# Optimization experiments

Hardware: AMD Instinct MI355X
Metric: run time of the kernel (lower is better)

Reference implementation:

```python
import jax, jax.numpy as jnp
import numpy as np

B, C, CI, H, W = 8, 256, 128, 64, 64
EPS = 1e-5


def conv1x1(x, w, b):
    # x: [B,C,H,W], w: [O,C], b: [O] -> [B,O,H,W]
    return jnp.einsum('bchw,oc->bohw', x, w) + b[None, :, None, None]


def maxpool2(x):
    # 2x2 max pool, stride 2 (NCHW)
    b, c, h, w = x.shape
    return x.reshape(b, c, h // 2, 2, w // 2, 2).max(axis=(3, 5))


def setup_inputs() -> dict:
    key = jax.random.key(0)
    ks = jax.random.split(key, 14)
    s_in = 1.0 / np.sqrt(C)
    s_ci = 1.0 / np.sqrt(CI)
    return {
        'x': jax.random.normal(ks[0], (B, C, H, W), jnp.float32),
        'w_theta': jax.random.normal(ks[1], (CI, C), jnp.float32) * s_in,
        'b_theta': jax.random.normal(ks[2], (CI,), jnp.float32) * 0.01,
        'w_phi': jax.random.normal(ks[3], (CI, C), jnp.float32) * s_in,
        'b_phi': jax.random.normal(ks[4], (CI,), jnp.float32) * 0.01,
        'w_g': jax.random.normal(ks[5], (CI, C), jnp.float32) * s_in,
        'b_g': jax.random.normal(ks[6], (CI,), jnp.float32) * 0.01,
        'w_w': jax.random.normal(ks[7], (C, CI), jnp.float32) * s_ci,
        'b_w': jax.random.normal(ks[8], (C,), jnp.float32) * 0.01,
        'bn_gamma': jax.random.normal(ks[9], (C,), jnp.float32) * 0.1,
        'bn_beta': jax.random.normal(ks[10], (C,), jnp.float32) * 0.1,
        'bn_mean': jax.random.normal(ks[11], (C,), jnp.float32) * 0.1,
        'bn_var': jax.random.uniform(ks[12], (C,), jnp.float32) + 0.5,
    }


def reference(x, w_theta, b_theta, w_phi, b_phi, w_g, b_g,
              w_w, b_w, bn_gamma, bn_beta, bn_mean, bn_var):
    b = x.shape[0]
    theta_x = conv1x1(x, w_theta, b_theta).reshape(b, CI, -1)            # [B,Ci,N]
    phi_x = maxpool2(conv1x1(x, w_phi, b_phi)).reshape(b, CI, -1)        # [B,Ci,M]
    g_x = maxpool2(conv1x1(x, w_g, b_g)).reshape(b, CI, -1)              # [B,Ci,M]
    m = phi_x.shape[-1]
    # unnormalized attention: f = theta^T phi / M  -> [B,N,M]
    f = jnp.einsum('bcn,bcm->bnm', theta_x, phi_x) / m
    y = jnp.einsum('bnm,bcm->bcn', f, g_x).reshape(b, CI, H, W)          # [B,Ci,H,W]
    w_y = conv1x1(y, w_w, b_w)                                           # [B,C,H,W]
    inv = jax.lax.rsqrt(bn_var + EPS)
    bn = (w_y - bn_mean[None, :, None, None]) * (bn_gamma * inv)[None, :, None, None] \
         + bn_beta[None, :, None, None]
    return bn + x
```

## Files before the change

kernel.cpp:

```cpp
#include <hip/hip_runtime.h>


typedef __attribute__((ext_vector_type(8))) short bf16x8;
typedef __attribute__((ext_vector_type(4))) float f32x4;
typedef unsigned short u16;
typedef unsigned int u32;

constexpr int Bn = 8, Cc = 256, CiC = 128, NnC = 4096, MmC = 1024;
constexpr float kEps = 1e-5f;

__device__ __forceinline__ u16 f2b(float f) {
  u32 u = __float_as_uint(f);
  return (u16)((u + 0x7fffu + ((u >> 16) & 1u)) >> 16);
}
__device__ __forceinline__ float b2f(u16 h) {
  return __uint_as_float(((u32)h) << 16);
}
__device__ __forceinline__ u32 pack2(float a, float b) {
  return (u32)f2b(a) | ((u32)f2b(b) << 16);
}
__device__ __forceinline__ void gl16(const void* g, void* l) {
  __builtin_amdgcn_global_load_lds(
      (const __attribute__((address_space(1))) void*)g,
      (__attribute__((address_space(3))) void*)l, 16, 0, 0);
}

__global__ __launch_bounds__(256) void prepw_kernel(
    const float* __restrict__ wt, const float* __restrict__ wp,
    const float* __restrict__ wg, const float* __restrict__ ww,
    u16* __restrict__ W3b, u16* __restrict__ Wwb) {
  const int idx = blockIdx.x * 256 + threadIdx.x;
  if (idx < 98304) {
    const int r = idx >> 8, c = idx & 255;
    const float v = (r < 128)   ? wt[r * 256 + c]
                    : (r < 256) ? wp[(r - 128) * 256 + c]
                                : wg[(r - 256) * 256 + c];
    W3b[idx] = f2b(v);
  } else {
    const int j = idx - 98304;
    Wwb[j] = f2b(ww[j]);
  }
}

__global__ __launch_bounds__(256) void prepx_kernel(const float* __restrict__ x,
                                                    u16* __restrict__ xT) {
  __shared__ float sm[64][65];
  const int b = blockIdx.z, c0 = blockIdx.y * 64, n0 = blockIdx.x * 64;
  const int tid = threadIdx.x;
  {
    const int n = tid & 63, cg = tid >> 6;
#pragma unroll
    for (int i = 0; i < 16; ++i) {
      const int c = cg * 16 + i;
      sm[c][n] = x[((size_t)(b * Cc + c0 + c)) * NnC + n0 + n];
    }
  }
  __syncthreads();
  {
    const int n = tid >> 2, q = tid & 3;
    u16 v[16];
#pragma unroll
    for (int j = 0; j < 16; ++j) v[j] = f2b(sm[q * 16 + j][n]);
    uint4 o0, o1;
    o0.x = v[0] | ((u32)v[1] << 16);
    o0.y = v[2] | ((u32)v[3] << 16);
    o0.z = v[4] | ((u32)v[5] << 16);
    o0.w = v[6] | ((u32)v[7] << 16);
    o1.x = v[8] | ((u32)v[9] << 16);
    o1.y = v[10] | ((u32)v[11] << 16);
    o1.z = v[12] | ((u32)v[13] << 16);
    o1.w = v[14] | ((u32)v[15] << 16);
    uint4* dst = (uint4*)(xT + ((size_t)(b * NnC + n0 + n)) * Cc + c0 + q * 16);
    dst[0] = o0;
    dst[1] = o1;
  }
}

__global__ __launch_bounds__(256) void conv3_kernel(
    const u16* __restrict__ xT, const u16* __restrict__ W3b,
    const float* __restrict__ b_theta, const float* __restrict__ b_phi,
    const float* __restrict__ b_g, u16* __restrict__ thetaT,
    u16* __restrict__ phiT, u16* __restrict__ gP) {
  __shared__ u16 sm[2][2][8192];
  const int mt = blockIdx.x, nt = blockIdx.y, b = blockIdx.z;
  const int n0 = nt * 128;
  const int tid = threadIdx.x;
  const int w = tid >> 6, lane = tid & 63;
  const int r16 = lane & 15, kg = lane >> 4;
  const int oh = (w & 1) * 64, nh = (w >> 1) * 64;

  auto stage = [&](int buf, int k0) {
#pragma unroll
    for (int i = 0; i < 4; ++i) {
      const int lin = i * 4096 + tid * 16;
      const int row = lin >> 7, byte = lin & 127;
      gl16((const char*)W3b + (size_t)(mt * 128 + row) * 512 + k0 * 2 +
               (byte ^ ((row & 7) << 4)),
           (char*)&sm[buf][0][0] + lin);
    }
#pragma unroll
    for (int i = 0; i < 4; ++i) {
      const int lin = i * 4096 + tid * 16;
      const int row = lin >> 7, byte = lin & 127;
      gl16((const char*)xT + ((size_t)(b * NnC + n0 + row) * Cc + k0) * 2 +
               (byte ^ ((row & 7) << 4)),
           (char*)&sm[buf][1][0] + lin);
    }
  };

  f32x4 acc[4][4];
#pragma unroll
  for (int i = 0; i < 4; ++i)
#pragma unroll
    for (int j = 0; j < 4; ++j) acc[i][j] = (f32x4)0.f;

  stage(0, 0);
  __syncthreads();
  for (int kt = 0; kt < 4; ++kt) {
    if (kt < 3) stage((kt + 1) & 1, (kt + 1) * 64);
    const char* A = (const char*)&sm[kt & 1][0][0];
    const char* Bm = (const char*)&sm[kt & 1][1][0];
#pragma unroll
    for (int ks = 0; ks < 2; ++ks) {
      bf16x8 af[4], bfr[4];
#pragma unroll
      for (int f = 0; f < 4; ++f) {
        const int o = oh + f * 16 + r16;
        af[f] = *(const bf16x8*)(A + ((o * 128 + ks * 64 + kg * 16) ^
                                      ((o & 7) << 4)));
        const int n = nh + f * 16 + r16;
        bfr[f] = *(const bf16x8*)(Bm + ((n * 128 + ks * 64 + kg * 16) ^
                                        ((n & 7) << 4)));
      }
#pragma unroll
      for (int fo = 0; fo < 4; ++fo)
#pragma unroll
        for (int fn = 0; fn < 4; ++fn)
          acc[fo][fn] = __builtin_amdgcn_mfma_f32_16x16x32_bf16(
              af[fo], bfr[fn], acc[fo][fn], 0, 0, 0);
    }
    __syncthreads();
  }

  const float* bias = (mt == 0) ? b_theta : (mt == 1) ? b_phi : b_g;
  u16* ldst = (u16*)&sm[0][0][0];
#pragma unroll
  for (int fo = 0; fo < 4; ++fo) {
    const int obase = oh + fo * 16 + kg * 4;
    const float b0 = bias[obase], b1 = bias[obase + 1], b2 = bias[obase + 2],
                b3 = bias[obase + 3];
#pragma unroll
    for (int fn = 0; fn < 4; ++fn) {
      const int n = nh + fn * 16 + r16;
      const f32x4 v = acc[fo][fn];
      uint2 p;
      p.x = pack2(v.x + b0, v.y + b1);
      p.y = pack2(v.z + b2, v.w + b3);
      *(uint2*)((char*)ldst + ((n * 256 + obase * 2) ^ ((n & 7) << 4))) = p;
    }
  }
  __syncthreads();

  if (mt == 0) {
#pragma unroll
    for (int i = 0; i < 8; ++i) {
      const int lin = i * 4096 + tid * 16;
      const int nl = lin >> 8, byte = lin & 255;
      const uint4 v =
          *(const uint4*)((const char*)ldst + ((nl * 256 + byte) ^ ((nl & 7) << 4)));
      *(uint4*)((char*)thetaT + (size_t)(b * NnC + n0 + nl) * CiC * 2 + byte) = v;
    }
  } else if (mt == 1) {
    const int ci = tid & 127, mg = tid >> 7;
#pragma unroll
    for (int i = 0; i < 16; ++i) {
      const int mw = mg * 16 + i;
      const int n00 = 2 * mw;
      float v0 = b2f(*(const u16*)((const char*)ldst +
                                   ((n00 * 256 + ci * 2) ^ ((n00 & 7) << 4))));
      float v1 = b2f(*(const u16*)((const char*)ldst +
                                   (((n00 + 1) * 256 + ci * 2) ^ (((n00 + 1) & 7) << 4))));
      float v2 = b2f(*(const u16*)((const char*)ldst +
                                   (((n00 + 64) * 256 + ci * 2) ^ (((n00 + 64) & 7) << 4))));
      float v3 = b2f(*(const u16*)((const char*)ldst +
                                   (((n00 + 65) * 256 + ci * 2) ^ (((n00 + 65) & 7) << 4))));
      const float mx = fmaxf(fmaxf(v0, v1), fmaxf(v2, v3));
      phiT[((size_t)(b * MmC + nt * 32 + mw)) * CiC + ci] = f2b(mx);
    }
  } else {
    const int ci = tid >> 1, half = tid & 1;
#pragma unroll
    for (int i = 0; i < 16; ++i) {
      const int mw = half * 16 + i;
      const int n00 = 2 * mw;
      float v0 = b2f(*(const u16*)((const char*)ldst +
                                   ((n00 * 256 + ci * 2) ^ ((n00 & 7) << 4))));
      float v1 = b2f(*(const u16*)((const char*)ldst +
                                   (((n00 + 1) * 256 + ci * 2) ^ (((n00 + 1) & 7) << 4))));
      float v2 = b2f(*(const u16*)((const char*)ldst +
                                   (((n00 + 64) * 256 + ci * 2) ^ (((n00 + 64) & 7) << 4))));
      float v3 = b2f(*(const u16*)((const char*)ldst +
                                   (((n00 + 65) * 256 + ci * 2) ^ (((n00 + 65) & 7) << 4))));
      const float mx = fmaxf(fmaxf(v0, v1), fmaxf(v2, v3));
      gP[((size_t)(b * CiC + ci)) * MmC + nt * 32 + mw] = f2b(mx);
    }
  }
}

__global__ __launch_bounds__(512) void attn_kernel(
    const u16* __restrict__ thetaT, const u16* __restrict__ phiT,
    const u16* __restrict__ gP, u16* __restrict__ yT) {
  __shared__ u16 thS[128 * 128];
  __shared__ u16 phS[2][64 * 128];
  __shared__ u16 gS[2][128 * 64];
  __shared__ u16 SP[128 * 64];
  const int nt = blockIdx.x, b = blockIdx.y;
  const int n0 = nt * 128;
  const int tid = threadIdx.x, w = tid >> 6, lane = tid & 63;
  const int r16 = lane & 15, kg = lane >> 4;

#pragma unroll
  for (int i = 0; i < 4; ++i) {
    const int lin = i * 8192 + tid * 16;
    const int nl = lin >> 8, byte = lin & 255;
    gl16((const char*)thetaT + (size_t)(b * NnC + n0 + nl) * CiC * 2 +
             (byte ^ ((nl & 7) << 4)),
         (char*)thS + lin);
  }
  auto stagePG = [&](int buf, int m0) {
#pragma unroll
    for (int i = 0; i < 2; ++i) {
      const int lin = i * 8192 + tid * 16;
      const int ml = lin >> 8, byte = lin & 255;
      gl16((const char*)phiT + (size_t)(b * MmC + m0 + ml) * CiC * 2 +
               (byte ^ ((ml & 7) << 4)),
           (char*)&phS[buf][0] + lin);
    }
#pragma unroll
    for (int i = 0; i < 2; ++i) {
      const int lin = i * 8192 + tid * 16;
      const int cil = lin >> 7, byte = lin & 127;
      gl16((const char*)gP + ((size_t)(b * CiC + cil) * MmC + m0) * 2 +
               (byte ^ ((cil & 7) << 4)),
           (char*)&gS[buf][0] + lin);
    }
  };
  stagePG(0, 0);
  __syncthreads();

  f32x4 accY[2][4];
#pragma unroll
  for (int i = 0; i < 2; ++i)
#pragma unroll
    for (int j = 0; j < 4; ++j) accY[i][j] = (f32x4)0.f;

  const int mrow = (w >> 1) * 16 + r16;
  const int nbs = (w & 1) * 64;
  const int mcb = (w >> 1) * 16 + kg * 4;
  const int cib = (w & 3) * 32;
  const int nb2 = (w >> 2) * 64;

  for (int mi = 0; mi < 16; ++mi) {
    const int cur = mi & 1;
    if (mi < 15) stagePG(cur ^ 1, (mi + 1) * 64);
    const char* ph = (const char*)&phS[cur][0];
    f32x4 s[4];
#pragma unroll
    for (int nf = 0; nf < 4; ++nf) s[nf] = (f32x4)0.f;
#pragma unroll
    for (int ks = 0; ks < 4; ++ks) {
      const bf16x8 af = *(const bf16x8*)(ph + ((mrow * 256 + ks * 64 + kg * 16) ^
                                               ((mrow & 7) << 4)));
#pragma unroll
      for (int nf = 0; nf < 4; ++nf) {
        const int n = nbs + nf * 16 + r16;
        const bf16x8 bf_ = *(const bf16x8*)((const char*)thS +
                                            ((n * 256 + ks * 64 + kg * 16) ^
                                             ((n & 7) << 4)));
        s[nf] = __builtin_amdgcn_mfma_f32_16x16x32_bf16(af, bf_, s[nf], 0, 0, 0);
      }
    }
#pragma unroll
    for (int nf = 0; nf < 4; ++nf) {
      const int n = nbs + nf * 16 + r16;
      uint2 p;
      p.x = pack2(s[nf].x, s[nf].y);
      p.y = pack2(s[nf].z, s[nf].w);
      *(uint2*)((char*)SP + ((n * 128 + mcb * 2) ^ ((n & 7) << 4))) = p;
    }
    __syncthreads();
    const char* gs = (const char*)&gS[cur][0];
#pragma unroll
    for (int ks2 = 0; ks2 < 2; ++ks2) {
      bf16x8 ga[2];
#pragma unroll
      for (int cf = 0; cf < 2; ++cf) {
        const int ci = cib + cf * 16 + r16;
        ga[cf] = *(const bf16x8*)(gs + ((ci * 128 + ks2 * 64 + kg * 16) ^
                                        ((ci & 7) << 4)));
      }
#pragma unroll
      for (int nf = 0; nf < 4; ++nf) {
        const int n = nb2 + nf * 16 + r16;
        const bf16x8 sb = *(const bf16x8*)((const char*)SP +
                                           ((n * 128 + ks2 * 64 + kg * 16) ^
                                            ((n & 7) << 4)));
#pragma unroll
        for (int cf = 0; cf < 2; ++cf)
          accY[cf][nf] = __builtin_amdgcn_mfma_f32_16x16x32_bf16(
              ga[cf], sb, accY[cf][nf], 0, 0, 0);
      }
    }
    __syncthreads();
  }

  constexpr float scl = 1.f / (float)MmC;
  u16* yt = thS;
#pragma unroll
  for (int cf = 0; cf < 2; ++cf) {
    const int c0 = cib + cf * 16 + kg * 4;
#pragma unroll
    for (int nf = 0; nf < 4; ++nf) {
      const int n = nb2 + nf * 16 + r16;
      const f32x4 v = accY[cf][nf];
      uint2 p;
      p.x = pack2(v.x * scl, v.y * scl);
      p.y = pack2(v.z * scl, v.w * scl);
      *(uint2*)((char*)yt + ((n * 256 + c0 * 2) ^ ((n & 7) << 4))) = p;
    }
  }
  __syncthreads();
#pragma unroll
  for (int i = 0; i < 4; ++i) {
    const int lin = i * 8192 + tid * 16;
    const int nl = lin >> 8, byte = lin & 255;
    const uint4 v =
        *(const uint4*)((const char*)yt + ((nl * 256 + byte) ^ ((nl & 7) << 4)));
    *(uint4*)((char*)yT + (size_t)(b * NnC + n0 + nl) * CiC * 2 + byte) = v;
  }
}

__global__ __launch_bounds__(256) void convw_kernel(
    const u16* __restrict__ yT, const u16* __restrict__ Wwb,
    const float* __restrict__ b_w, const float* __restrict__ gamma,
    const float* __restrict__ beta, const float* __restrict__ mean,
    const float* __restrict__ var, const float* __restrict__ x,
    float* __restrict__ out) {
  __shared__ u16 smA[128 * 128];
  __shared__ u16 smB[128 * 128];
  __shared__ float scs[128], offs[128];
  const int mt = blockIdx.x, nt = blockIdx.y, b = blockIdx.z;
  const int n0 = nt * 128, tid = threadIdx.x;
  const int w = tid >> 6, lane = tid & 63;
  const int r16 = lane & 15, kg = lane >> 4;
  if (tid < 128) {
    const int o = mt * 128 + tid;
    const float sc = gamma[o] * rsqrtf(var[o] + kEps);
    scs[tid] = sc;
    offs[tid] = beta[o] + (b_w[o] - mean[o]) * sc;
  }
#pragma unroll
  for (int i = 0; i < 8; ++i) {
    const int lin = i * 4096 + tid * 16;
    const int row = lin >> 8, byte = lin & 255;
    gl16((const char*)Wwb + (size_t)(mt * 128 + row) * 256 +
             (byte ^ ((row & 7) << 4)),
         (char*)smA + lin);
    gl16((const char*)yT + (size_t)(b * NnC + n0 + row) * 256 +
             (byte ^ ((row & 7) << 4)),
         (char*)smB + lin);
  }
  __syncthreads();

  f32x4 acc[4][4];
#pragma unroll
  for (int i = 0; i < 4; ++i)
#pragma unroll
    for (int j = 0; j < 4; ++j) acc[i][j] = (f32x4)0.f;
  const int oh = (w & 1) * 64, nh = (w >> 1) * 64;
#pragma unroll
  for (int ks = 0; ks < 4; ++ks) {
    bf16x8 af[4], bfr[4];
#pragma unroll
    for (int f = 0; f < 4; ++f) {
      const int o = oh + f * 16 + r16;
      af[f] = *(const bf16x8*)((const char*)smA +
                               ((o * 256 + ks * 64 + kg * 16) ^ ((o & 7) << 4)));
      const int n = nh + f * 16 + r16;
      bfr[f] = *(const bf16x8*)((const char*)smB +
                                ((n * 256 + ks * 64 + kg * 16) ^ ((n & 7) << 4)));
    }
#pragma unroll
    for (int fo = 0; fo < 4; ++fo)
#pragma unroll
      for (int fn = 0; fn < 4; ++fn)
        acc[fo][fn] = __builtin_amdgcn_mfma_f32_16x16x32_bf16(
            af[fo], bfr[fn], acc[fo][fn], 0, 0, 0);
  }

  const size_t xb = ((size_t)b * Cc + mt * 128) * NnC;
#pragma unroll
  for (int fo = 0; fo < 4; ++fo) {
#pragma unroll
    for (int r = 0; r < 4; ++r) {
      const int ol = oh + fo * 16 + kg * 4 + r;
      const float sc = scs[ol], of = offs[ol];
      const size_t rowoff = xb + (size_t)ol * NnC + n0;
#pragma unroll
      for (int fn = 0; fn < 4; ++fn) {
        const int n = nh + fn * 16 + r16;
        out[rowoff + n] = fmaf(acc[fo][fn][r], sc, of) + x[rowoff + n];
      }
    }
  }
}

extern "C" void kernel_launch(void* const* d_in, const int* in_sizes, int n_in,
                              void* d_out, int out_size, void* d_ws,
                              size_t ws_size, hipStream_t stream) {
  const float* x = (const float*)d_in[0];
  const float* w_theta = (const float*)d_in[1];
  const float* b_theta = (const float*)d_in[2];
  const float* w_phi = (const float*)d_in[3];
  const float* b_phi = (const float*)d_in[4];
  const float* w_g = (const float*)d_in[5];
  const float* b_g = (const float*)d_in[6];
  const float* w_w = (const float*)d_in[7];
  const float* b_w = (const float*)d_in[8];
  const float* bn_gamma = (const float*)d_in[9];
  const float* bn_beta = (const float*)d_in[10];
  const float* bn_mean = (const float*)d_in[11];
  const float* bn_var = (const float*)d_in[12];
  float* out = (float*)d_out;

  char* ws = (char*)d_ws;
  u16* xT = (u16*)ws;
  u16* thetaT = (u16*)(ws + 16777216);
  u16* phiT = (u16*)(ws + 25165824);
  u16* gP = (u16*)(ws + 27262976);
  u16* yT = (u16*)(ws + 29360128);
  u16* W3b = (u16*)(ws + 37748736);
  u16* Wwb = (u16*)(ws + 37945344);
  if (ws_size < 38010880ull) return;

  prepw_kernel<<<dim3(512), dim3(256), 0, stream>>>(w_theta, w_phi, w_g, w_w,
                                                    W3b, Wwb);
  prepx_kernel<<<dim3(64, 4, 8), dim3(256), 0, stream>>>(x, xT);
  conv3_kernel<<<dim3(3, 32, 8), dim3(256), 0, stream>>>(
      xT, W3b, b_theta, b_phi, b_g, thetaT, phiT, gP);
  attn_kernel<<<dim3(32, 8), dim3(512), 0, stream>>>(thetaT, phiT, gP, yT);
  convw_kernel<<<dim3(2, 32, 8), dim3(256), 0, stream>>>(
      yT, Wwb, b_w, bn_gamma, bn_beta, bn_mean, bn_var, x, out);
}
```

Baseline: 165.0 us.

## Reassociate linear attention into per-batch folded weight matrix applied to x

```diff
diff --git a/kernel.cpp b/kernel.cpp
--- a/kernel.cpp
+++ b/kernel.cpp
@@ -6,7 +6,7 @@
 typedef unsigned short u16;
 typedef unsigned int u32;
 
-constexpr int Bn = 8, Cc = 256, CiC = 128, NnC = 4096, MmC = 1024;
+constexpr int Cc = 256, NnC = 4096;
 constexpr float kEps = 1e-5f;
 
 __device__ __forceinline__ u16 f2b(float f) {
@@ -26,20 +26,11 @@
 }
 
 __global__ __launch_bounds__(256) void prepw_kernel(
-    const float* __restrict__ wt, const float* __restrict__ wp,
-    const float* __restrict__ wg, const float* __restrict__ ww,
-    u16* __restrict__ W3b, u16* __restrict__ Wwb) {
+    const float* __restrict__ wp, const float* __restrict__ wg,
+    u16* __restrict__ Wfg) {
   const int idx = blockIdx.x * 256 + threadIdx.x;
-  if (idx < 98304) {
-    const int r = idx >> 8, c = idx & 255;
-    const float v = (r < 128)   ? wt[r * 256 + c]
-                    : (r < 256) ? wp[(r - 128) * 256 + c]
-                                : wg[(r - 256) * 256 + c];
-    W3b[idx] = f2b(v);
-  } else {
-    const int j = idx - 98304;
-    Wwb[j] = f2b(ww[j]);
-  }
+  const int r = idx >> 8, c = idx & 255;
+  Wfg[idx] = f2b(r < 128 ? wp[r * 256 + c] : wg[(r - 128) * 256 + c]);
 }
 
 __global__ __launch_bounds__(256) void prepx_kernel(const float* __restrict__ x,
@@ -76,11 +67,10 @@
   }
 }
 
-__global__ __launch_bounds__(256) void conv3_kernel(
-    const u16* __restrict__ xT, const u16* __restrict__ W3b,
-    const float* __restrict__ b_theta, const float* __restrict__ b_phi,
-    const float* __restrict__ b_g, u16* __restrict__ thetaT,
-    u16* __restrict__ phiT, u16* __restrict__ gP) {
+__global__ __launch_bounds__(256) void convfg_kernel(
+    const u16* __restrict__ xT, const u16* __restrict__ Wfg,
+    const float* __restrict__ b_phi, const float* __restrict__ b_g,
+    u16* __restrict__ phiT, u16* __restrict__ gT) {
   __shared__ u16 sm[2][2][8192];
   const int mt = blockIdx.x, nt = blockIdx.y, b = blockIdx.z;
   const int n0 = nt * 128;
@@ -94,7 +84,7 @@
     for (int i = 0; i < 4; ++i) {
       const int lin = i * 4096 + tid * 16;
       const int row = lin >> 7, byte = lin & 127;
-      gl16((const char*)W3b + (size_t)(mt * 128 + row) * 512 + k0 * 2 +
+      gl16((const char*)Wfg + (size_t)(mt * 128 + row) * 512 + k0 * 2 +
                (byte ^ ((row & 7) << 4)),
            (char*)&sm[buf][0][0] + lin);
     }
@@ -142,7 +132,7 @@
     __syncthreads();
   }
 
-  const float* bias = (mt == 0) ? b_theta : (mt == 1) ? b_phi : b_g;
+  const float* bias = (mt == 0) ? b_phi : b_g;
   u16* ldst = (u16*)&sm[0][0][0];
 #pragma unroll
   for (int fo = 0; fo < 4; ++fo) {
@@ -161,241 +151,242 @@
   }
   __syncthreads();
 
-  if (mt == 0) {
+  u16* dst = (mt == 0) ? phiT : gT;
+  const int ci = tid >> 1, half = tid & 1;
+#pragma unroll
+  for (int i = 0; i < 16; ++i) {
+    const int mw = half * 16 + i;
+    const int n00 = 2 * mw;
+    float v0 = b2f(*(const u16*)((const char*)ldst +
+                                 ((n00 * 256 + ci * 2) ^ ((n00 & 7) << 4))));
+    float v1 = b2f(*(const u16*)((const char*)ldst +
+                                 (((n00 + 1) * 256 + ci * 2) ^ (((n00 + 1) & 7) << 4))));
+    float v2 = b2f(*(const u16*)((const char*)ldst +
+                                 (((n00 + 64) * 256 + ci * 2) ^ (((n00 + 64) & 7) << 4))));
+    float v3 = b2f(*(const u16*)((const char*)ldst +
+                                 (((n00 + 65) * 256 + ci * 2) ^ (((n00 + 65) & 7) << 4))));
+    const float mx = fmaxf(fmaxf(v0, v1), fmaxf(v2, v3));
+    dst[((size_t)(b * 128 + ci)) * 1024 + nt * 32 + mw] = f2b(mx);
+  }
+}
+
+__global__ __launch_bounds__(256) void g2_kernel(const u16* __restrict__ phiT,
+                                                 const u16* __restrict__ gT,
+                                                 float* __restrict__ A_g2) {
+  __shared__ u16 sm[2][12288];
+  const int ch0 = blockIdx.x * 64, b = blockIdx.y;
+  const int tid = threadIdx.x;
+  const int w = tid >> 6, lane = tid & 63;
+  const int r16 = lane & 15, kg = lane >> 4;
+  const int cih = (w & 1) * 64, cch = (w >> 1) * 32;
+
+  auto stage = [&](int buf, int m0) {
+#pragma unroll
+    for (int i = 0; i < 4; ++i) {
+      const int lin = i * 4096 + tid * 16;
+      const int row = lin >> 7, byte = lin & 127;
+      gl16((const char*)gT + ((size_t)(b * 128 + row) * 1024 + m0) * 2 +
+               (byte ^ ((row & 7) << 4)),
+           (char*)&sm[buf][0] + lin);
+    }
+#pragma unroll
+    for (int i = 0; i < 2; ++i) {
+      const int lin = i * 4096 + tid * 16;
+      const int row = lin >> 7, byte = lin & 127;
+      gl16((const char*)phiT + ((size_t)(b * 128 + ch0 + row) * 1024 + m0) * 2 +
+               (byte ^ ((row & 7) << 4)),
+           (char*)&sm[buf][8192] + lin);
+    }
+  };
+
+  f32x4 acc[4][2];
+#pragma unroll
+  for (int i = 0; i < 4; ++i)
+#pragma unroll
+    for (int j = 0; j < 2; ++j) acc[i][j] = (f32x4)0.f;
+
+  stage(0, 0);
+  __syncthreads();
+  for (int kt = 0; kt < 16; ++kt) {
+    if (kt < 15) stage((kt + 1) & 1, (kt + 1) * 64);
+    const char* A = (const char*)&sm[kt & 1][0];
+    const char* Bp = A + 16384;
+#pragma unroll
+    for (int ks = 0; ks < 2; ++ks) {
+      bf16x8 af[4], bfr[2];
+#pragma unroll
+      for (int f = 0; f < 4; ++f) {
+        const int o = cih + f * 16 + r16;
+        af[f] = *(const bf16x8*)(A + ((o * 128 + ks * 64 + kg * 16) ^
+                                      ((o & 7) << 4)));
+      }
+#pragma unroll
+      for (int f = 0; f < 2; ++f) {
+        const int lc = cch + f * 16 + r16;
+        bfr[f] = *(const bf16x8*)(Bp + ((lc * 128 + ks * 64 + kg * 16) ^
+                                        ((lc & 7) << 4)));
+      }
+#pragma unroll
+      for (int fo = 0; fo < 4; ++fo)
+#pragma unroll
+        for (int fn = 0; fn < 2; ++fn)
+          acc[fo][fn] = __builtin_amdgcn_mfma_f32_16x16x32_bf16(
+              af[fo], bfr[fn], acc[fo][fn], 0, 0, 0);
+    }
+    __syncthreads();
+  }
+
+  constexpr float scl = 1.f / 1024.f;
+#pragma unroll
+  for (int fo = 0; fo < 4; ++fo) {
+#pragma unroll
+    for (int r = 0; r < 4; ++r) {
+      const int ci = cih + fo * 16 + kg * 4 + r;
+#pragma unroll
+      for (int fn = 0; fn < 2; ++fn) {
+        const int c = ch0 + cch + fn * 16 + r16;
+        A_g2[(size_t)b * 16384 + ci * 128 + c] = acc[fo][fn][r] * scl;
+      }
+    }
+  }
+}
+
+__global__ __launch_bounds__(256) void t1_kernel(const float* __restrict__ A_g2,
+                                                 const float* __restrict__ w_theta,
+                                                 float* __restrict__ T1) {
+  __shared__ float As[16][128];
+  __shared__ float Ws[128][17];
+  const int tile = blockIdx.x, b = blockIdx.y;
+  const int ci0 = (tile >> 4) * 16, j0 = (tile & 15) * 16;
+  const int t = threadIdx.x;
+#pragma unroll
+  for (int i = 0; i < 8; ++i) {
+    const int idx = t + i * 256;
+    As[idx >> 7][idx & 127] =
+        A_g2[(size_t)b * 16384 + (ci0 + (idx >> 7)) * 128 + (idx & 127)];
+    Ws[idx >> 4][idx & 15] = w_theta[(idx >> 4) * 256 + j0 + (idx & 15)];
+  }
+  __syncthreads();
+  const int tci = t >> 4, tj = t & 15;
+  float s = 0.f;
+#pragma unroll 8
+  for (int c = 0; c < 128; ++c) s = fmaf(As[tci][c], Ws[c][tj], s);
+  T1[(size_t)b * 32768 + (ci0 + tci) * 256 + j0 + tj] = s;
+}
+
+__global__ __launch_bounds__(256) void wbig_kernel(
+    const float* __restrict__ T1, const float* __restrict__ A_g2,
+    const float* __restrict__ w_w, const float* __restrict__ b_theta,
+    const float* __restrict__ b_w, u16* __restrict__ Wbig,
+    float* __restrict__ beff) {
+  __shared__ float Ws2[16][128];
+  __shared__ float T1s[128][17];
+  __shared__ float v1[128];
+  const int tile = blockIdx.x, b = blockIdx.y;
+  const int t = threadIdx.x;
+  if (tile < 256) {
+    const int o0 = (tile >> 4) * 16, j0 = (tile & 15) * 16;
 #pragma unroll
     for (int i = 0; i < 8; ++i) {
-      const int lin = i * 4096 + tid * 16;
-      const int nl = lin >> 8, byte = lin & 255;
-      const uint4 v =
-          *(const uint4*)((const char*)ldst + ((nl * 256 + byte) ^ ((nl & 7) << 4)));
-      *(uint4*)((char*)thetaT + (size_t)(b * NnC + n0 + nl) * CiC * 2 + byte) = v;
-    }
-  } else if (mt == 1) {
-    const int ci = tid & 127, mg = tid >> 7;
-#pragma unroll
-    for (int i = 0; i < 16; ++i) {
-      const int mw = mg * 16 + i;
-      const int n00 = 2 * mw;
-      float v0 = b2f(*(const u16*)((const char*)ldst +
-                                   ((n00 * 256 + ci * 2) ^ ((n00 & 7) << 4))));
-      float v1 = b2f(*(const u16*)((const char*)ldst +
-                                   (((n00 + 1) * 256 + ci * 2) ^ (((n00 + 1) & 7) << 4))));
-      float v2 = b2f(*(const u16*)((const char*)ldst +
-                                   (((n00 + 64) * 256 + ci * 2) ^ (((n00 + 64) & 7) << 4))));
-      float v3 = b2f(*(const u16*)((const char*)ldst +
-                                   (((n00 + 65) * 256 + ci * 2) ^ (((n00 + 65) & 7) << 4))));
-      const float mx = fmaxf(fmaxf(v0, v1), fmaxf(v2, v3));
-      phiT[((size_t)(b * MmC + nt * 32 + mw)) * CiC + ci] = f2b(mx);
-    }
+      const int idx = t + i * 256;
+      Ws2[idx >> 7][idx & 127] = w_w[(o0 + (idx >> 7)) * 128 + (idx & 127)];
+      T1s[idx >> 4][idx & 15] =
+          T1[(size_t)b * 32768 + (idx >> 4) * 256 + j0 + (idx & 15)];
+    }
+    __syncthreads();
+    const int to = t >> 4, tj = t & 15;
+    float s = 0.f;
+#pragma unroll 8
+    for (int c = 0; c < 128; ++c) s = fmaf(Ws2[to][c], T1s[c][tj], s);
+    Wbig[(size_t)b * 65536 + (o0 + to) * 256 + j0 + tj] = f2b(s);
   } else {
-    const int ci = tid >> 1, half = tid & 1;
-#pragma unroll
-    for (int i = 0; i < 16; ++i) {
-      const int mw = half * 16 + i;
-      const int n00 = 2 * mw;
-      float v0 = b2f(*(const u16*)((const char*)ldst +
-                                   ((n00 * 256 + ci * 2) ^ ((n00 & 7) << 4))));
-      float v1 = b2f(*(const u16*)((const char*)ldst +
-                                   (((n00 + 1) * 256 + ci * 2) ^ (((n00 + 1) & 7) << 4))));
-      float v2 = b2f(*(const u16*)((const char*)ldst +
-                                   (((n00 + 64) * 256 + ci * 2) ^ (((n00 + 64) & 7) << 4))));
-      float v3 = b2f(*(const u16*)((const char*)ldst +
-                                   (((n00 + 65) * 256 + ci * 2) ^ (((n00 + 65) & 7) << 4))));
-      const float mx = fmaxf(fmaxf(v0, v1), fmaxf(v2, v3));
-      gP[((size_t)(b * CiC + ci)) * MmC + nt * 32 + mw] = f2b(mx);
-    }
-  }
-}
-
-__global__ __launch_bounds__(512) void attn_kernel(
-    const u16* __restrict__ thetaT, const u16* __restrict__ phiT,
-    const u16* __restrict__ gP, u16* __restrict__ yT) {
-  __shared__ u16 thS[128 * 128];
-  __shared__ u16 phS[2][64 * 128];
-  __shared__ u16 gS[2][128 * 64];
-  __shared__ u16 SP[128 * 64];
-  const int nt = blockIdx.x, b = blockIdx.y;
-  const int n0 = nt * 128;
-  const int tid = threadIdx.x, w = tid >> 6, lane = tid & 63;
-  const int r16 = lane & 15, kg = lane >> 4;
-
-#pragma unroll
-  for (int i = 0; i < 4; ++i) {
-    const int lin = i * 8192 + tid * 16;
-    const int nl = lin >> 8, byte = lin & 255;
-    gl16((const char*)thetaT + (size_t)(b * NnC + n0 + nl) * CiC * 2 +
-             (byte ^ ((nl & 7) << 4)),
-         (char*)thS + lin);
-  }
-  auto stagePG = [&](int buf, int m0) {
-#pragma unroll
-    for (int i = 0; i < 2; ++i) {
-      const int lin = i * 8192 + tid * 16;
-      const int ml = lin >> 8, byte = lin & 255;
-      gl16((const char*)phiT + (size_t)(b * MmC + m0 + ml) * CiC * 2 +
-               (byte ^ ((ml & 7) << 4)),
-           (char*)&phS[buf][0] + lin);
-    }
-#pragma unroll
-    for (int i = 0; i < 2; ++i) {
-      const int lin = i * 8192 + tid * 16;
-      const int cil = lin >> 7, byte = lin & 127;
-      gl16((const char*)gP + ((size_t)(b * CiC + cil) * MmC + m0) * 2 +
-               (byte ^ ((cil & 7) << 4)),
-           (char*)&gS[buf][0] + lin);
-    }
-  };
-  stagePG(0, 0);
-  __syncthreads();
-
-  f32x4 accY[2][4];
-#pragma unroll
-  for (int i = 0; i < 2; ++i)
-#pragma unroll
-    for (int j = 0; j < 4; ++j) accY[i][j] = (f32x4)0.f;
-
-  const int mrow = (w >> 1) * 16 + r16;
-  const int nbs = (w & 1) * 64;
-  const int mcb = (w >> 1) * 16 + kg * 4;
-  const int cib = (w & 3) * 32;
-  const int nb2 = (w >> 2) * 64;
-
-  for (int mi = 0; mi < 16; ++mi) {
-    const int cur = mi & 1;
-    if (mi < 15) stagePG(cur ^ 1, (mi + 1) * 64);
-    const char* ph = (const char*)&phS[cur][0];
-    f32x4 s[4];
-#pragma unroll
-    for (int nf = 0; nf < 4; ++nf) s[nf] = (f32x4)0.f;
-#pragma unroll
-    for (int ks = 0; ks < 4; ++ks) {
-      const bf16x8 af = *(const bf16x8*)(ph + ((mrow * 256 + ks * 64 + kg * 16) ^
-                                               ((mrow & 7) << 4)));
-#pragma unroll
-      for (int nf = 0; nf < 4; ++nf) {
-        const int n = nbs + nf * 16 + r16;
-        const bf16x8 bf_ = *(const bf16x8*)((const char*)thS +
-                                            ((n * 256 + ks * 64 + kg * 16) ^
-                                             ((n & 7) << 4)));
-        s[nf] = __builtin_amdgcn_mfma_f32_16x16x32_bf16(af, bf_, s[nf], 0, 0, 0);
-      }
-    }
-#pragma unroll
-    for (int nf = 0; nf < 4; ++nf) {
-      const int n = nbs + nf * 16 + r16;
-      uint2 p;
-      p.x = pack2(s[nf].x, s[nf].y);
-      p.y = pack2(s[nf].z, s[nf].w);
-      *(uint2*)((char*)SP + ((n * 128 + mcb * 2) ^ ((n & 7) << 4))) = p;
+    if (t < 128) {
+      float s = 0.f;
+      for (int c = 0; c < 128; ++c)
+        s = fmaf(A_g2[(size_t)b * 16384 + t * 128 + c], b_theta[c], s);
+      v1[t] = s;
     }
     __syncthreads();
-    const char* gs = (const char*)&gS[cur][0];
-#pragma unroll
-    for (int ks2 = 0; ks2 < 2; ++ks2) {
-      bf16x8 ga[2];
-#pragma unroll
-      for (int cf = 0; cf < 2; ++cf) {
-        const int ci = cib + cf * 16 + r16;
-        ga[cf] = *(const bf16x8*)(gs + ((ci * 128 + ks2 * 64 + kg * 16) ^
-                                        ((ci & 7) << 4)));
-      }
-#pragma unroll
-      for (int nf = 0; nf < 4; ++nf) {
-        const int n = nb2 + nf * 16 + r16;
-        const bf16x8 sb = *(const bf16x8*)((const char*)SP +
-                                           ((n * 128 + ks2 * 64 + kg * 16) ^
-                                            ((n & 7) << 4)));
-#pragma unroll
-        for (int cf = 0; cf < 2; ++cf)
-          accY[cf][nf] = __builtin_amdgcn_mfma_f32_16x16x32_bf16(
-              ga[cf], sb, accY[cf][nf], 0, 0, 0);
-      }
-    }
-    __syncthreads();
-  }
-
-  constexpr float scl = 1.f / (float)MmC;
-  u16* yt = thS;
-#pragma unroll
-  for (int cf = 0; cf < 2; ++cf) {
-    const int c0 = cib + cf * 16 + kg * 4;
-#pragma unroll
-    for (int nf = 0; nf < 4; ++nf) {
-      const int n = nb2 + nf * 16 + r16;
-      const f32x4 v = accY[cf][nf];
-      uint2 p;
-      p.x = pack2(v.x * scl, v.y * scl);
-      p.y = pack2(v.z * scl, v.w * scl);
-      *(uint2*)((char*)yt + ((n * 256 + c0 * 2) ^ ((n & 7) << 4))) = p;
-    }
-  }
-  __syncthreads();
-#pragma unroll
-  for (int i = 0; i < 4; ++i) {
-    const int lin = i * 8192 + tid * 16;
-    const int nl = lin >> 8, byte = lin & 255;
-    const uint4 v =
-        *(const uint4*)((const char*)yt + ((nl * 256 + byte) ^ ((nl & 7) << 4)));
-    *(uint4*)((char*)yT + (size_t)(b * NnC + n0 + nl) * CiC * 2 + byte) = v;
-  }
-}
-
-__global__ __launch_bounds__(256) void convw_kernel(
-    const u16* __restrict__ yT, const u16* __restrict__ Wwb,
-    const float* __restrict__ b_w, const float* __restrict__ gamma,
+    float s2 = b_w[t];
+    for (int ci = 0; ci < 128; ++ci) s2 = fmaf(w_w[t * 128 + ci], v1[ci], s2);
+    beff[b * 256 + t] = s2;
+  }
+}
+
+__global__ __launch_bounds__(256) void final_kernel(
+    const u16* __restrict__ xT, const u16* __restrict__ Wbig,
+    const float* __restrict__ beff, const float* __restrict__ gamma,
     const float* __restrict__ beta, const float* __restrict__ mean,
     const float* __restrict__ var, const float* __restrict__ x,
     float* __restrict__ out) {
-  __shared__ u16 smA[128 * 128];
-  __shared__ u16 smB[128 * 128];
+  __shared__ u16 sm[2][2][8192];
   __shared__ float scs[128], offs[128];
   const int mt = blockIdx.x, nt = blockIdx.y, b = blockIdx.z;
-  const int n0 = nt * 128, tid = threadIdx.x;
+  const int n0 = nt * 128;
+  const int tid = threadIdx.x;
   const int w = tid >> 6, lane = tid & 63;
   const int r16 = lane & 15, kg = lane >> 4;
+  const int oh = (w & 1) * 64, nh = (w >> 1) * 64;
+
   if (tid < 128) {
     const int o = mt * 128 + tid;
     const float sc = gamma[o] * rsqrtf(var[o] + kEps);
     scs[tid] = sc;
-    offs[tid] = beta[o] + (b_w[o] - mean[o]) * sc;
-  }
-#pragma unroll
-  for (int i = 0; i < 8; ++i) {
-    const int lin = i * 4096 + tid * 16;
-    const int row = lin >> 8, byte = lin & 255;
-    gl16((const char*)Wwb + (size_t)(mt * 128 + row) * 256 +
-             (byte ^ ((row & 7) << 4)),
-         (char*)smA + lin);
-    gl16((const char*)yT + (size_t)(b * NnC + n0 + row) * 256 +
-             (byte ^ ((row & 7) << 4)),
-         (char*)smB + lin);
-  }
-  __syncthreads();
+    offs[tid] = beta[o] + (beff[b * 256 + o] - mean[o]) * sc;
+  }
+
+  auto stage = [&](int buf, int k0) {
+#pragma unroll
+    for (int i = 0; i < 4; ++i) {
+      const int lin = i * 4096 + tid * 16;
+      const int row = lin >> 7, byte = lin & 127;
+      gl16((const char*)Wbig + (size_t)b * 131072 +
+               (size_t)(mt * 128 + row) * 512 + k0 * 2 +
+               (byte ^ ((row & 7) << 4)),
+           (char*)&sm[buf][0][0] + lin);
+    }
+#pragma unroll
+    for (int i = 0; i < 4; ++i) {
+      const int lin = i * 4096 + tid * 16;
+      const int row = lin >> 7, byte = lin & 127;
+      gl16((const char*)xT + ((size_t)(b * NnC + n0 + row) * Cc + k0) * 2 +
+               (byte ^ ((row & 7) << 4)),
+           (char*)&sm[buf][1][0] + lin);
+    }
+  };
 
   f32x4 acc[4][4];
 #pragma unroll
   for (int i = 0; i < 4; ++i)
 #pragma unroll
     for (int j = 0; j < 4; ++j) acc[i][j] = (f32x4)0.f;
-  const int oh = (w & 1) * 64, nh = (w >> 1) * 64;
-#pragma unroll
-  for (int ks = 0; ks < 4; ++ks) {
-    bf16x8 af[4], bfr[4];
-#pragma unroll
-    for (int f = 0; f < 4; ++f) {
-      const int o = oh + f * 16 + r16;
-      af[f] = *(const bf16x8*)((const char*)smA +
-                               ((o * 256 + ks * 64 + kg * 16) ^ ((o & 7) << 4)));
-      const int n = nh + f * 16 + r16;
-      bfr[f] = *(const bf16x8*)((const char*)smB +
-                                ((n * 256 + ks * 64 + kg * 16) ^ ((n & 7) << 4)));
-    }
-#pragma unroll
-    for (int fo = 0; fo < 4; ++fo)
-#pragma unroll
-      for (int fn = 0; fn < 4; ++fn)
-        acc[fo][fn] = __builtin_amdgcn_mfma_f32_16x16x32_bf16(
-            af[fo], bfr[fn], acc[fo][fn], 0, 0, 0);
+
+  stage(0, 0);
+  __syncthreads();
+  for (int kt = 0; kt < 4; ++kt) {
+    if (kt < 3) stage((kt + 1) & 1, (kt + 1) * 64);
+    const char* A = (const char*)&sm[kt & 1][0][0];
+    const char* Bm = (const char*)&sm[kt & 1][1][0];
+#pragma unroll
+    for (int ks = 0; ks < 2; ++ks) {
+      bf16x8 af[4], bfr[4];
+#pragma unroll
+      for (int f = 0; f < 4; ++f) {
+        const int o = oh + f * 16 + r16;
+        af[f] = *(const bf16x8*)(A + ((o * 128 + ks * 64 + kg * 16) ^
+                                      ((o & 7) << 4)));
+        const int n = nh + f * 16 + r16;
+        bfr[f] = *(const bf16x8*)(Bm + ((n * 128 + ks * 64 + kg * 16) ^
+                                        ((n & 7) << 4)));
+      }
+#pragma unroll
+      for (int fo = 0; fo < 4; ++fo)
+#pragma unroll
+        for (int fn = 0; fn < 4; ++fn)
+          acc[fo][fn] = __builtin_amdgcn_mfma_f32_16x16x32_bf16(
+              af[fo], bfr[fn], acc[fo][fn], 0, 0, 0);
+    }
+    __syncthreads();
   }
 
   const size_t xb = ((size_t)b * Cc + mt * 128) * NnC;
@@ -435,20 +426,23 @@
 
   char* ws = (char*)d_ws;
   u16* xT = (u16*)ws;
-  u16* thetaT = (u16*)(ws + 16777216);
-  u16* phiT = (u16*)(ws + 25165824);
-  u16* gP = (u16*)(ws + 27262976);
-  u16* yT = (u16*)(ws + 29360128);
-  u16* W3b = (u16*)(ws + 37748736);
-  u16* Wwb = (u16*)(ws + 37945344);
-  if (ws_size < 38010880ull) return;
-
-  prepw_kernel<<<dim3(512), dim3(256), 0, stream>>>(w_theta, w_phi, w_g, w_w,
-                                                    W3b, Wwb);
+  u16* Wfg = (u16*)(ws + 16777216);
+  u16* phiT = (u16*)(ws + 16908288);
+  u16* gT = (u16*)(ws + 19005440);
+  float* A_g2 = (float*)(ws + 21102592);
+  float* T1 = (float*)(ws + 21626880);
+  u16* Wbig = (u16*)(ws + 22675456);
+  float* beff = (float*)(ws + 23724032);
+  if (ws_size < 23732224ull) return;
+
+  prepw_kernel<<<dim3(256), dim3(256), 0, stream>>>(w_phi, w_g, Wfg);
   prepx_kernel<<<dim3(64, 4, 8), dim3(256), 0, stream>>>(x, xT);
-  conv3_kernel<<<dim3(3, 32, 8), dim3(256), 0, stream>>>(
-      xT, W3b, b_theta, b_phi, b_g, thetaT, phiT, gP);
-  attn_kernel<<<dim3(32, 8), dim3(512), 0, stream>>>(thetaT, phiT, gP, yT);
-  convw_kernel<<<dim3(2, 32, 8), dim3(256), 0, stream>>>(
-      yT, Wwb, b_w, bn_gamma, bn_beta, bn_mean, bn_var, x, out);
-}
+  convfg_kernel<<<dim3(2, 32, 8), dim3(256), 0, stream>>>(
+      xT, Wfg, b_phi, b_g, phiT, gT);
+  g2_kernel<<<dim3(2, 8), dim3(256), 0, stream>>>(phiT, gT, A_g2);
+  t1_kernel<<<dim3(128, 8), dim3(256), 0, stream>>>(A_g2, w_theta, T1);
+  wbig_kernel<<<dim3(257, 8), dim3(256), 0, stream>>>(T1, A_g2, w_w, b_theta,
+                                                      b_w, Wbig, beff);
+  final_kernel<<<dim3(2, 32, 8), dim3(256), 0, stream>>>(
+      xT, Wbig, beff, bn_gamma, bn_beta, bn_mean, bn_var, x, out);
+}
```

Measured after the change: 157.6 us. 1.05x faster.
